# Performance work log

Hardware: AMD Instinct MI355X
Metric: run time of the kernel (lower is better)

The kernel has to match this reference:

```python
import jax, jax.numpy as jnp
import numpy as np
from jax import lax

B, S, D, N, K = 4, 8192, 128, 2, 3
G = N + 1  # n_order + 1 projection groups
EPS_L1 = 1e-8


def _theta(d):
    # RoPE inverse frequencies: 10000^{-2i/d}
    return 1.0 / (10000.0 ** (jnp.arange(d // 2, dtype=jnp.float32) * 2.0 / d))


def _rope(x, pos, theta):
    # x: (B,S,D), pos: (B,S) int -> dimension-wise 2x2 rotations
    ang = pos[..., None].astype(jnp.float32) * theta  # (B,S,D/2)
    c, s = jnp.cos(ang), jnp.sin(ang)
    xe, xo = x[..., 0::2], x[..., 1::2]
    return jnp.stack([xe * c - xo * s, xe * s + xo * c], axis=-1).reshape(x.shape)


def _layernorm(x, g, b, eps=1e-5):
    mu = jnp.mean(x, axis=-1, keepdims=True)
    var = jnp.var(x, axis=-1, keepdims=True)
    return (x - mu) / jnp.sqrt(var + eps) * g + b


def _fft_long_conv(v, h):
    # torch norm='forward': rfft divides by n, irfft does not -> circular conv / (2L)
    L = v.shape[-1]
    n = 2 * L
    V = jnp.fft.rfft(v, n=n, norm='forward')
    H = jnp.fft.rfft(h, n=n, norm='forward')
    return jnp.fft.irfft(V * H, n=n, norm='forward')[..., :L]


def setup_inputs() -> dict:
    key = jax.random.key(0)
    ks = jax.random.split(key, 8)
    sc = lambda fan_in: (2.0 / fan_in) ** 0.5
    return {
        'embeddings': jax.random.normal(ks[0], (B, S, D), dtype=jnp.float32),
        'W_proj': jax.random.normal(ks[1], (D, G * D), dtype=jnp.float32) * sc(D),
        'conv_w': jax.random.normal(ks[2], (G * D, 1, K), dtype=jnp.float32) * sc(K),
        'conv_b': jnp.zeros((G * D,), dtype=jnp.float32),
        'W1': jax.random.normal(ks[3], (D, D), dtype=jnp.float32) * sc(D),
        'b1': jnp.zeros((D,), dtype=jnp.float32),
        'ln_g': jnp.ones((D,), dtype=jnp.float32),
        'ln_b': jnp.zeros((D,), dtype=jnp.float32),
        'W2': jax.random.normal(ks[4], (D, N * D), dtype=jnp.float32) * sc(D),
        'b2': jnp.zeros((N * D,), dtype=jnp.float32),
        'ff_scale': jnp.ones((1, 1, N * D), dtype=jnp.float32),
        'out_proj': jax.random.normal(ks[5], (D, D), dtype=jnp.float32) * sc(D),
        'B_param': jax.random.normal(ks[6], (N, 1, D, 1), dtype=jnp.float32) * sc(D),
        'positions': (jnp.arange(B * S, dtype=jnp.int32).reshape(B, S) % S),
    }


def reference(embeddings, W_proj, conv_w, conv_b, W1, b1, ln_g, ln_b, W2, b2,
              ff_scale, out_proj, B_param, positions):
    theta = _theta(D)
    # --- HyenaProjection: dense proj + fully-depthwise short conv ---
    x = embeddings @ W_proj                      # (B,S,G*D)
    xc = jnp.transpose(x, (0, 2, 1))             # (B,G*D,S)
    z = lax.conv_general_dilated(
        xc, conv_w, (1,), [(K // 2, K // 2)],
        dimension_numbers=('NCH', 'OIH', 'NCH'),
        feature_group_count=G * D) + conv_b[None, :, None]
    # faithful to torch: (B,S,G*D) row-major reshape into (B,D,G,S)
    z = jnp.transpose(z, (0, 2, 1)).reshape(B, D, G, S)
    z_list = [z[:, :, i, :] for i in range(G)]   # each (B,D,S)
    # --- HyenaFilter: RoPE + FFN + L1 normalization over emb dim ---
    t = _rope(embeddings, positions, theta)
    hmid = jax.nn.gelu(_layernorm(t @ W1 + b1, ln_g, ln_b), approximate=False)
    h_hat = (hmid @ W2 + b2) * ff_scale          # (B,S,N*D)
    h_hat = jnp.transpose(h_hat.reshape(B, S, N, D), (0, 2, 3, 1))  # (B,N,D,S)
    h_hat = h_hat / (jnp.sum(jnp.abs(h_hat), axis=-2, keepdims=True) + EPS_L1)
    # --- Hyena recurrence with FFT long conv ---
    v = z_list[-1]
    for i in range(N):
        v = z_list[i] * (_fft_long_conv(v, h_hat[:, i]) + B_param[i] * v)
    out = jnp.transpose(v, (0, 2, 1)) @ out_proj  # (B,S,D)
    return out
```

## Files before the change

### kernel.cpp

```cpp
#include <hip/hip_runtime.h>
#include <hip/hip_bf16.h>
#include <cstdint>

#define BB 4
#define SS 8192
#define DD 128

#define N_EMB  4194304
#define N_WP   49152
#define N_CW   1152
#define N_CB   384
#define N_W1   16384
#define N_B1   128
#define N_LNG  128
#define N_LNB  128
#define N_W2   32768
#define N_B2   256
#define N_FFS  256
#define N_WO   16384
#define N_BP   256
#define N_FINP 4311680

typedef short bf16x8 __attribute__((ext_vector_type(8)));
typedef float f32x4  __attribute__((ext_vector_type(4)));

__device__ __forceinline__ void bfsplit(float v, unsigned short& h, unsigned short& l)
{
    __hip_bfloat16 hb = __float2bfloat16(v);
    float hf = __bfloat162float(hb);
    __hip_bfloat16 lb = __float2bfloat16(v - hf);
    h = *(unsigned short*)&hb;
    l = *(unsigned short*)&lb;
}

__device__ __forceinline__ void packAB(const float* __restrict__ src, bf16x8& H, bf16x8& L)
{
    float4 x0 = *(const float4*)(src);
    float4 x1 = *(const float4*)(src + 4);
    float xv[8] = {x0.x, x0.y, x0.z, x0.w, x1.x, x1.y, x1.z, x1.w};
    unsigned short h[8], l[8];
    #pragma unroll
    for (int j = 0; j < 8; ++j) bfsplit(xv[j], h[j], l[j]);
    #pragma unroll
    for (int j = 0; j < 8; ++j) { H[j] = (short)h[j]; L[j] = (short)l[j]; }
}

struct SrcPtrs { const void* p[13]; };

__device__ __forceinline__ float readf(const void* p, int idx, bool isbf)
{
    if (isbf) return __uint_as_float(((unsigned)((const unsigned short*)p)[idx]) << 16);
    return ((const float*)p)[idx];
}

__global__ __launch_bounds__(256) void k_convert(
    SrcPtrs sp, float* __restrict__ dst,
    unsigned short* __restrict__ embh, unsigned short* __restrict__ embl,
    unsigned short* __restrict__ wpth, unsigned short* __restrict__ wptl,
    unsigned short* __restrict__ w1th, unsigned short* __restrict__ w1tl,
    unsigned short* __restrict__ w2th, unsigned short* __restrict__ w2tl,
    unsigned short* __restrict__ woth, unsigned short* __restrict__ wotl)
{
    static const int sizes[13] = {N_EMB, N_WP, N_CW, N_CB, N_W1, N_B1, N_LNG,
                                  N_LNB, N_W2, N_B2, N_FFS, N_WO, N_BP};
    const unsigned probe = *(const unsigned*)sp.p[6];
    const bool isbf = (probe != 0x3F800000u);
    const int gid = blockIdx.x * 256 + threadIdx.x;
    const int stride = gridDim.x * 256;
    int off = 0;
    for (int seg = 0; seg < 13; ++seg) {
        const int n = sizes[seg];
        float* d = dst + off;
        for (int i = gid; i < n; i += stride) {
            float v = readf(sp.p[seg], i, isbf);
            d[i] = v;
            if (seg == 0) { unsigned short h, l; bfsplit(v, h, l); embh[i] = h; embl[i] = l; }
        }
        off += n;
    }
    for (int i = gid; i < N_WP; i += stride) {
        int n = i >> 7, k = i & 127;
        unsigned short h, l; bfsplit(readf(sp.p[1], k * 384 + n, isbf), h, l);
        wpth[i] = h; wptl[i] = l;
    }
    for (int i = gid; i < N_W1; i += stride) {
        int n = i >> 7, k = i & 127;
        unsigned short h, l; bfsplit(readf(sp.p[4], k * 128 + n, isbf), h, l);
        w1th[i] = h; w1tl[i] = l;
    }
    for (int i = gid; i < N_W2; i += stride) {
        int n = i >> 7, k = i & 127;
        unsigned short h, l; bfsplit(readf(sp.p[8], k * 256 + n, isbf), h, l);
        w2th[i] = h; w2tl[i] = l;
    }
    for (int i = gid; i < N_WO; i += stride) {
        int n = i >> 7, k = i & 127;
        unsigned short h, l; bfsplit(readf(sp.p[11], k * 128 + n, isbf), h, l);
        woth[i] = h; wotl[i] = l;
    }
}

#define PCROWS 112

__global__ __launch_bounds__(512) void k_projconv(
    const unsigned short* __restrict__ embh,
    const unsigned short* __restrict__ embl,
    const unsigned short* __restrict__ wpth,
    const unsigned short* __restrict__ wptl,
    const float* __restrict__ cw,
    const float* __restrict__ cb,
    float* __restrict__ zbuf)
{
    __shared__ float xs[128][68];

    const int b    = blockIdx.y;
    const int s0   = blockIdx.x * PCROWS;
    const int t    = threadIdx.x;
    const int wv   = t >> 6;
    const int lane = t & 63;
    const int m    = lane & 15;
    const int q    = lane >> 4;

    bf16x8 Ah[4], Al[4];
    {
        int sx  = s0 - 8 + 16 * wv + m;
        int sxc = min(max(sx, 0), SS - 1);
        const size_t rowoff = ((size_t)b * SS + sxc) * DD;
        #pragma unroll
        for (int kt = 0; kt < 4; ++kt) {
            int k0 = kt * 32 + q * 8;
            Ah[kt] = *(const bf16x8*)(embh + rowoff + k0);
            Al[kt] = *(const bf16x8*)(embl + rowoff + k0);
        }
    }

    for (int nc = 0; nc < 6; ++nc) {
        #pragma unroll
        for (int nt = 0; nt < 4; ++nt) {
            int n = nc * 64 + nt * 16 + m;
            const size_t noff = (size_t)n * DD;
            f32x4 acc = {0.f, 0.f, 0.f, 0.f};
            #pragma unroll
            for (int kt = 0; kt < 4; ++kt) {
                int k0 = kt * 32 + q * 8;
                bf16x8 Bh = *(const bf16x8*)(wpth + noff + k0);
                bf16x8 Bl = *(const bf16x8*)(wptl + noff + k0);
                acc = __builtin_amdgcn_mfma_f32_16x16x32_bf16(Ah[kt], Bh, acc, 0, 0, 0);
                acc = __builtin_amdgcn_mfma_f32_16x16x32_bf16(Ah[kt], Bl, acc, 0, 0, 0);
                acc = __builtin_amdgcn_mfma_f32_16x16x32_bf16(Al[kt], Bh, acc, 0, 0, 0);
            }
            #pragma unroll
            for (int rg = 0; rg < 4; ++rg)
                xs[16 * wv + 4 * q + rg][nt * 16 + m] = acc[rg];
        }
        __syncthreads();
        {
            int c = t & 63, rg = t >> 6;
            int ch = nc * 64 + c;
            float w0 = cw[ch * 3 + 0], w1 = cw[ch * 3 + 1], w2 = cw[ch * 3 + 2];
            float bias = cb[ch];
            #pragma unroll
            for (int i = 0; i < 14; ++i) {
                int r = rg + 8 * i;
                int s = s0 + r;
                if (s < SS) {
                    float x0 = (s > 0)      ? xs[r + 7][c] : 0.f;
                    float x1 = xs[r + 8][c];
                    float x2 = (s < SS - 1) ? xs[r + 9][c] : 0.f;
                    zbuf[((size_t)b * SS + s) * 384 + ch] = x0 * w0 + x1 * w1 + x2 * w2 + bias;
                }
            }
        }
        __syncthreads();
    }
}

__global__ __launch_bounds__(256) void k_mlp(
    const float* __restrict__ emb,
    const int* __restrict__ positions,
    const unsigned short* __restrict__ w1th,
    const unsigned short* __restrict__ w1tl,
    const float* __restrict__ b1,
    const float* __restrict__ ln_g,
    const float* __restrict__ ln_b,
    const unsigned short* __restrict__ w2th,
    const unsigned short* __restrict__ w2tl,
    const float* __restrict__ b2,
    const float* __restrict__ ffs,
    float* __restrict__ hhat)
{
    const int b  = blockIdx.y;
    const int s0 = blockIdx.x * 16;
    const int t  = threadIdx.x;
    __shared__ float tls[16][132];
    __shared__ float hls[16][132];
    __shared__ float hh[16][257];
    __shared__ float rstat[16][2];

    for (int idx = t; idx < 16 * 64; idx += 256) {
        int r = idx >> 6, i = idx & 63;
        int s = s0 + r;
        const float2 p = ((const float2*)(emb + ((size_t)b * SS + s) * DD))[i];
        float xe = p.x, xo = p.y;
        float pos = (float)positions[(size_t)b * SS + s];
        float th = exp2f((float)i * (-13.287712379549449f / 64.0f));
        float ang = pos * th;
        float sn, cs;
        sincosf(ang, &sn, &cs);
        tls[r][2 * i]     = xe * cs - xo * sn;
        tls[r][2 * i + 1] = xe * sn + xo * cs;
    }
    __syncthreads();

    const int wv = t >> 6, lane = t & 63, m = lane & 15, q = lane >> 4;

    {
        bf16x8 Ah[4], Al[4];
        #pragma unroll
        for (int kt = 0; kt < 4; ++kt)
            packAB(&tls[m][kt * 32 + q * 8], Ah[kt], Al[kt]);
        #pragma unroll
        for (int ntl = 0; ntl < 2; ++ntl) {
            int nt = 2 * wv + ntl;
            int col = nt * 16 + m;
            const size_t noff = (size_t)col * 128;
            f32x4 acc = {0.f, 0.f, 0.f, 0.f};
            #pragma unroll
            for (int kt = 0; kt < 4; ++kt) {
                int k0 = kt * 32 + q * 8;
                bf16x8 Bh = *(const bf16x8*)(w1th + noff + k0);
                bf16x8 Bl = *(const bf16x8*)(w1tl + noff + k0);
                acc = __builtin_amdgcn_mfma_f32_16x16x32_bf16(Ah[kt], Bh, acc, 0, 0, 0);
                acc = __builtin_amdgcn_mfma_f32_16x16x32_bf16(Ah[kt], Bl, acc, 0, 0, 0);
                acc = __builtin_amdgcn_mfma_f32_16x16x32_bf16(Al[kt], Bh, acc, 0, 0, 0);
            }
            float bias = b1[col];
            #pragma unroll
            for (int rg = 0; rg < 4; ++rg)
                hls[4 * q + rg][col] = acc[rg] + bias;
        }
    }
    __syncthreads();

    {
        for (int r = wv; r < 16; r += 4) {
            float x0 = hls[r][lane], x1 = hls[r][lane + 64];
            float sum = x0 + x1, ssq = x0 * x0 + x1 * x1;
            #pragma unroll
            for (int off = 32; off > 0; off >>= 1) {
                sum += __shfl_xor(sum, off);
                ssq += __shfl_xor(ssq, off);
            }
            float mu  = sum * (1.0f / 128.0f);
            float var = ssq * (1.0f / 128.0f) - mu * mu;
            float inv = rsqrtf(var + 1e-5f);
            float y0 = (x0 - mu) * inv * ln_g[lane]      + ln_b[lane];
            float y1 = (x1 - mu) * inv * ln_g[lane + 64] + ln_b[lane + 64];
            hls[r][lane]      = y0 * 0.5f * (1.0f + erff(y0 * 0.70710678118654752f));
            hls[r][lane + 64] = y1 * 0.5f * (1.0f + erff(y1 * 0.70710678118654752f));
        }
    }
    __syncthreads();

    {
        bf16x8 Ah[4], Al[4];
        #pragma unroll
        for (int kt = 0; kt < 4; ++kt)
            packAB(&hls[m][kt * 32 + q * 8], Ah[kt], Al[kt]);
        #pragma unroll
        for (int ntl = 0; ntl < 4; ++ntl) {
            int nt = 4 * wv + ntl;
            int col = nt * 16 + m;
            const size_t noff = (size_t)col * 128;
            f32x4 acc = {0.f, 0.f, 0.f, 0.f};
            #pragma unroll
            for (int kt = 0; kt < 4; ++kt) {
                int k0 = kt * 32 + q * 8;
                bf16x8 Bh = *(const bf16x8*)(w2th + noff + k0);
                bf16x8 Bl = *(const bf16x8*)(w2tl + noff + k0);
                acc = __builtin_amdgcn_mfma_f32_16x16x32_bf16(Ah[kt], Bh, acc, 0, 0, 0);
                acc = __builtin_amdgcn_mfma_f32_16x16x32_bf16(Ah[kt], Bl, acc, 0, 0, 0);
                acc = __builtin_amdgcn_mfma_f32_16x16x32_bf16(Al[kt], Bh, acc, 0, 0, 0);
            }
            float bias = b2[col];
            float fsc  = ffs[col];
            #pragma unroll
            for (int rg = 0; rg < 4; ++rg)
                hh[4 * q + rg][col] = (acc[rg] + bias) * fsc;
        }
    }
    __syncthreads();

    {
        for (int g = wv; g < 32; g += 4) {
            int r = g >> 1, n = g & 1;
            float a = fabsf(hh[r][n * 128 + lane]) + fabsf(hh[r][n * 128 + lane + 64]);
            #pragma unroll
            for (int off = 32; off > 0; off >>= 1) a += __shfl_xor(a, off);
            if (lane == 0) rstat[r][n] = 1.0f / (a + 1e-8f);
        }
    }
    __syncthreads();

    for (int idx = t; idx < 16 * 256; idx += 256) {
        int nd = idx >> 4, rr = idx & 15;
        int n = nd >> 7;
        float val = hh[rr][nd] * rstat[rr][n];
        hhat[((size_t)(b * 2 + n) * 128 + (nd & 127)) * SS + (s0 + rr)] = val;
    }
}

__device__ __forceinline__ int SK(int x) { return x + (x >> 5); }

__global__ __launch_bounds__(1024) void k_fftconv(
    const float* __restrict__ zbuf,
    const float* __restrict__ hhat,
    const float* __restrict__ Bp,
    float* __restrict__ vout)
{
    const int d = blockIdx.x;
    const int b = blockIdx.y;
    const int t = threadIdx.x;
    __shared__ float lre[4224];
    __shared__ float lim[4224];
    __shared__ float2 twF[1280];

    const float c8 = 0.923879532511287f, s8 = 0.382683432365090f, c4 = 0.707106781186548f;

    {
        const int lhs_c[5] = {9, 7, 5, 3, 1};
        for (int idx = t; idx < 1280; idx += 1024) {
            int si = idx >> 8, jj = idx & 255;
            float sn, cs;
            sincospif((float)jj * (-1.0f / (float)(1 << lhs_c[si])), &sn, &cs);
            twF[idx] = make_float2(cs, sn);
        }
    }

    const float* zb = zbuf + (size_t)b * (SS * 384);
    const float* v0 = zb + ((size_t)d * 3 + 2) * SS;
    float vr[8];
    #pragma unroll
    for (int j = 0; j < 8; ++j) vr[j] = v0[t + j * 1024];

    float cre[16], cim[16];
    const float sc = 1.0f / 536870912.0f;
    const int blk = t >> 8, w = t & 255;
    __syncthreads();

    for (int it = 0; it < 2; ++it) {
        const float* hp = hhat + (((size_t)b * 2 + it) * 128 + d) * SS;
        #pragma unroll
        for (int j = 0; j < 8; ++j) { cre[j] = vr[j]; cim[j] = hp[t + j * 1024]; }

        {
            float W0i, W0r; sincospif((float)t * (-1.0f / 8192.0f), &W0i, &W0r);
            const float wjr[4] = {1.f, c8, c4, s8};
            const float wji[4] = {0.f, -s8, -c4, -c8};
            #pragma unroll
            for (int j = 0; j < 4; ++j) {
                float Wr = W0r * wjr[j] - W0i * wji[j];
                float Wi = W0r * wji[j] + W0i * wjr[j];
                float W2r = Wr * Wr - Wi * Wi, W2i = 2.f * Wr * Wi;
                float W3r = W2r * Wr - W2i * Wi, W3i = W2r * Wi + W2i * Wr;
                float a0r = cre[j], a0i = cim[j], a1r = cre[j + 4], a1i = cim[j + 4];
                cre[j] = a0r + a1r; cim[j] = a0i + a1i;
                float dr = a0r - a1r, di = a0i - a1i;
                cre[j + 4] = W2r * dr - W2i * di; cim[j + 4] = W2r * di + W2i * dr;
                float e2r = a0r + a1i, e2i = a0i - a1r;
                cre[j + 8] = Wr * e2r - Wi * e2i; cim[j + 8] = Wr * e2i + Wi * e2r;
                float e3r = a0r - a1i, e3i = a0i + a1r;
                cre[j + 12] = W3r * e3r - W3i * e3i; cim[j + 12] = W3r * e3i + W3i * e3r;
            }
        }
        {
            float Wi, Wr; sincospif((float)t * (-1.0f / 2048.0f), &Wi, &Wr);
            float W2r = Wr * Wr - Wi * Wi, W2i = 2.f * Wr * Wi;
            float W3r = W2r * Wr - W2i * Wi, W3i = W2r * Wi + W2i * Wr;
            #pragma unroll
            for (int g = 0; g < 16; g += 4) {
                float a0r = cre[g], a0i = cim[g], a1r = cre[g + 1], a1i = cim[g + 1];
                float a2r = cre[g + 2], a2i = cim[g + 2], a3r = cre[g + 3], a3i = cim[g + 3];
                float s02r = a0r + a2r, s02i = a0i + a2i, d02r = a0r - a2r, d02i = a0i - a2i;
                float s13r = a1r + a3r, s13i = a1i + a3i, d13r = a1r - a3r, d13i = a1i - a3i;
                cre[g] = s02r + s13r; cim[g] = s02i + s13i;
                float u1r = s02r - s13r, u1i = s02i - s13i;
                cre[g + 1] = W2r * u1r - W2i * u1i; cim[g + 1] = W2r * u1i + W2i * u1r;
                float e2r = d02r + d13i, e2i = d02i - d13r;
                cre[g + 2] = Wr * e2r - Wi * e2i; cim[g + 2] = Wr * e2i + Wi * e2r;
                float e3r = d02r - d13i, e3i = d02i + d13r;
                cre[g + 3] = W3r * e3r - W3i * e3i; cim[g + 3] = W3r * e3i + W3i * e3r;
            }
        }
        #pragma unroll
        for (int p = 0; p < 4; ++p) {
            #pragma unroll
            for (int q = 0; q < 4; ++q) {
                int a = SK(q * 1024 + t);
                lre[a] = cre[4 * p + q]; lim[a] = cim[4 * p + q];
            }
            __syncthreads();
            const int lhs_c[5] = {9, 7, 5, 3, 1};
            #pragma unroll
            for (int si = 0; si < 5; ++si) {
                const int lh = lhs_c[si];
                const int hh = 1 << lh, h2 = hh >> 1;
                const int jj = w & (h2 - 1);
                const int i0 = blk * 1024 + ((w >> (lh - 1)) << (lh + 1)) + jj;
                const float2 wv = twF[si * 256 + jj];
                const float Wr = wv.x, Wi = wv.y;
                const int p0 = SK(i0), p1 = SK(i0 + h2), p2 = SK(i0 + hh), p3 = SK(i0 + hh + h2);
                float a0r = lre[p0], a0i = lim[p0];
                float a1r = lre[p1], a1i = lim[p1];
                float a2r = lre[p2], a2i = lim[p2];
                float a3r = lre[p3], a3i = lim[p3];
                float W2r = Wr * Wr - Wi * Wi, W2i = 2.f * Wr * Wi;
                float W3r = W2r * Wr - W2i * Wi, W3i = W2r * Wi + W2i * Wr;
                float s02r = a0r + a2r, s02i = a0i + a2i, d02r = a0r - a2r, d02i = a0i - a2i;
                float s13r = a1r + a3r, s13i = a1i + a3i, d13r = a1r - a3r, d13i = a1i - a3i;
                lre[p0] = s02r + s13r; lim[p0] = s02i + s13i;
                float u1r = s02r - s13r, u1i = s02i - s13i;
                lre[p1] = W2r * u1r - W2i * u1i; lim[p1] = W2r * u1i + W2i * u1r;
                float e2r = d02r + d13i, e2i = d02i - d13r;
                lre[p2] = Wr * e2r - Wi * e2i; lim[p2] = Wr * e2i + Wi * e2r;
                float e3r = d02r - d13i, e3i = d02i + d13r;
                lre[p3] = W3r * e3r - W3i * e3i; lim[p3] = W3r * e3i + W3i * e3r;
                __syncthreads();
            }
            #pragma unroll
            for (int q = 0; q < 4; ++q) {
                int a = SK(q * 1024 + t);
                cre[4 * p + q] = lre[a]; cim[4 * p + q] = lim[a];
            }
            __syncthreads();
        }

        #pragma unroll
        for (int j = 0; j < 16; ++j) {
            float Cr = cre[j], Ci = cim[j];
            cre[j] = (Cr * Cr - Ci * Ci) * sc;
            cim[j] = 2.0f * Cr * Ci * sc;
        }

        #pragma unroll
        for (int p = 0; p < 4; ++p) {
            #pragma unroll
            for (int q = 0; q < 4; ++q) {
                int a = SK(q * 1024 + t);
                lre[a] = cre[4 * p + q]; lim[a] = cim[4 * p + q];
            }
            __syncthreads();
            const int lqs_c[5] = {0, 2, 4, 6, 8};
            #pragma unroll
            for (int si = 0; si < 5; ++si) {
                const int lq = lqs_c[si];
                const int qv = 1 << lq;
                const int jj = w & (qv - 1);
                const int i0 = blk * 1024 + ((w >> lq) << (lq + 2)) + jj;
                const float2 wv = twF[(4 - si) * 256 + jj];
                const float Wbr = wv.x, Wbi = -wv.y;
                const int p0 = SK(i0), p1 = SK(i0 + qv), p2 = SK(i0 + 2 * qv), p3 = SK(i0 + 3 * qv);
                float a0r = lre[p0], a0i = lim[p0];
                float a1r = lre[p1], a1i = lim[p1];
                float a2r = lre[p2], a2i = lim[p2];
                float a3r = lre[p3], a3i = lim[p3];
                float War = Wbr * Wbr - Wbi * Wbi, Wai = 2.f * Wbr * Wbi;
                float t1r = War * a1r - Wai * a1i, t1i = War * a1i + Wai * a1r;
                float b0r = a0r + t1r, b0i = a0i + t1i, b1r = a0r - t1r, b1i = a0i - t1i;
                float t3r = War * a3r - Wai * a3i, t3i = War * a3i + Wai * a3r;
                float b2r = a2r + t3r, b2i = a2i + t3i, b3r = a2r - t3r, b3i = a2i - t3i;
                float u2r = Wbr * b2r - Wbi * b2i, u2i = Wbr * b2i + Wbi * b2r;
                lre[p0] = b0r + u2r; lim[p0] = b0i + u2i;
                lre[p2] = b0r - u2r; lim[p2] = b0i - u2i;
                float u3r = -Wbi * b3r - Wbr * b3i, u3i = Wbr * b3r - Wbi * b3i;
                lre[p1] = b1r + u3r; lim[p1] = b1i + u3i;
                lre[p3] = b1r - u3r; lim[p3] = b1i - u3i;
                __syncthreads();
            }
            #pragma unroll
            for (int q = 0; q < 4; ++q) {
                int a = SK(q * 1024 + t);
                cre[4 * p + q] = lre[a]; cim[4 * p + q] = lim[a];
            }
            __syncthreads();
        }
        {
            float Wbi, Wbr; sincospif((float)t * (1.0f / 2048.0f), &Wbi, &Wbr);
            float War = Wbr * Wbr - Wbi * Wbi, Wai = 2.f * Wbr * Wbi;
            #pragma unroll
            for (int g = 0; g < 16; g += 4) {
                float a0r = cre[g], a0i = cim[g], a1r = cre[g + 1], a1i = cim[g + 1];
                float a2r = cre[g + 2], a2i = cim[g + 2], a3r = cre[g + 3], a3i = cim[g + 3];
                float t1r = War * a1r - Wai * a1i, t1i = War * a1i + Wai * a1r;
                float b0r = a0r + t1r, b0i = a0i + t1i, b1r = a0r - t1r, b1i = a0i - t1i;
                float t3r = War * a3r - Wai * a3i, t3i = War * a3i + Wai * a3r;
                float b2r = a2r + t3r, b2i = a2i + t3i, b3r = a2r - t3r, b3i = a2i - t3i;
                float u2r = Wbr * b2r - Wbi * b2i, u2i = Wbr * b2i + Wbi * b2r;
                cre[g] = b0r + u2r; cim[g] = b0i + u2i;
                cre[g + 2] = b0r - u2r; cim[g + 2] = b0i - u2i;
                float u3r = -Wbi * b3r - Wbr * b3i, u3i = Wbr * b3r - Wbi * b3i;
                cre[g + 1] = b1r + u3r; cim[g + 1] = b1i + u3i;
                cre[g + 3] = b1r - u3r; cim[g + 3] = b1i - u3i;
            }
        }
        {
            float Bi, Br; sincospif((float)t * (1.0f / 8192.0f), &Bi, &Br);
            const float bjr[4] = {1.f, c8, c4, s8};
            const float bji[4] = {0.f, s8, c4, c8};
            #pragma unroll
            for (int j = 0; j < 4; ++j) {
                float Wbr = Br * bjr[j] - Bi * bji[j];
                float Wbi = Br * bji[j] + Bi * bjr[j];
                float War = Wbr * Wbr - Wbi * Wbi, Wai = 2.f * Wbr * Wbi;
                float a0r = cre[j], a0i = cim[j], a1r = cre[j + 4], a1i = cim[j + 4];
                float a2r = cre[j + 8], a2i = cim[j + 8], a3r = cre[j + 12], a3i = cim[j + 12];
                float t1r = War * a1r - Wai * a1i, t1i = War * a1i + Wai * a1r;
                float b0r = a0r + t1r, b0i = a0i + t1i, b1r = a0r - t1r, b1i = a0i - t1i;
                float t3r = War * a3r - Wai * a3i, t3i = War * a3i + Wai * a3r;
                float b2r = a2r + t3r, b2i = a2i + t3i, b3r = a2r - t3r, b3i = a2i - t3i;
                float u2r = Wbr * b2r - Wbi * b2i, u2i = Wbr * b2i + Wbi * b2r;
                cre[j] = b0r + u2r; cim[j] = b0i + u2i;
                cre[j + 8] = b0r - u2r; cim[j + 8] = b0i - u2i;
                float u3r = -Wbi * b3r - Wbr * b3i, u3i = Wbr * b3r - Wbi * b3i;
                cre[j + 4] = b1r + u3r; cim[j + 4] = b1i + u3i;
                cre[j + 12] = b1r - u3r; cim[j + 12] = b1i - u3i;
            }
        }

        const float* zi = zb + ((size_t)d * 3 + it) * SS;
        const float bpv = Bp[it * 128 + d];
        #pragma unroll
        for (int j = 0; j < 8; ++j) {
            float zz = zi[t + j * 1024];
            vr[j] = zz * (cim[j] + bpv * vr[j]);
        }
        __syncthreads();
    }

    float* vo = vout + ((size_t)b * 128 + d) * SS;
    #pragma unroll
    for (int j = 0; j < 8; ++j) vo[t + j * 1024] = vr[j];
}

__global__ __launch_bounds__(256) void k_outproj(
    const float* __restrict__ vbuf,
    const unsigned short* __restrict__ woth,
    const unsigned short* __restrict__ wotl,
    const unsigned* __restrict__ probe,
    void* __restrict__ outv)
{
    __shared__ float vt[128 * 65];
    const int b  = blockIdx.y;
    const int s0 = blockIdx.x * 64;
    const int t  = threadIdx.x;
    for (int idx = t; idx < 8192; idx += 256) {
        int dd = idx >> 6, sl = idx & 63;
        vt[dd * 65 + sl] = vbuf[((size_t)b * 128 + dd) * SS + s0 + sl];
    }
    const bool isbf = (*probe != 0x3F800000u);
    __syncthreads();

    const int wv = t >> 6, lane = t & 63, m = lane & 15, q = lane >> 4;

    bf16x8 Ah[4], Al[4];
    #pragma unroll
    for (int kt = 0; kt < 4; ++kt) {
        float xv[8];
        unsigned short h[8], l[8];
        #pragma unroll
        for (int j = 0; j < 8; ++j) {
            int dd = kt * 32 + q * 8 + j;
            xv[j] = vt[dd * 65 + 16 * wv + m];
        }
        #pragma unroll
        for (int j = 0; j < 8; ++j) bfsplit(xv[j], h[j], l[j]);
        #pragma unroll
        for (int j = 0; j < 8; ++j) { Ah[kt][j] = (short)h[j]; Al[kt][j] = (short)l[j]; }
    }

    f32x4 acc[8];
    #pragma unroll
    for (int nt = 0; nt < 8; ++nt) {
        acc[nt] = (f32x4){0.f, 0.f, 0.f, 0.f};
        const size_t noff = (size_t)(nt * 16 + m) * 128;
        #pragma unroll
        for (int kt = 0; kt < 4; ++kt) {
            int k0 = kt * 32 + q * 8;
            bf16x8 Bh = *(const bf16x8*)(woth + noff + k0);
            bf16x8 Bl = *(const bf16x8*)(wotl + noff + k0);
            acc[nt] = __builtin_amdgcn_mfma_f32_16x16x32_bf16(Ah[kt], Bh, acc[nt], 0, 0, 0);
            acc[nt] = __builtin_amdgcn_mfma_f32_16x16x32_bf16(Ah[kt], Bl, acc[nt], 0, 0, 0);
            acc[nt] = __builtin_amdgcn_mfma_f32_16x16x32_bf16(Al[kt], Bh, acc[nt], 0, 0, 0);
        }
    }

    if (isbf) {
        __hip_bfloat16* out = (__hip_bfloat16*)outv;
        #pragma unroll
        for (int nt = 0; nt < 8; ++nt)
            #pragma unroll
            for (int rg = 0; rg < 4; ++rg) {
                int s = s0 + 16 * wv + 4 * q + rg;
                out[((size_t)b * SS + s) * DD + nt * 16 + m] = __float2bfloat16(acc[nt][rg]);
            }
    } else {
        float* out = (float*)outv;
        #pragma unroll
        for (int nt = 0; nt < 8; ++nt)
            #pragma unroll
            for (int rg = 0; rg < 4; ++rg) {
                int s = s0 + 16 * wv + 4 * q + rg;
                out[((size_t)b * SS + s) * DD + nt * 16 + m] = acc[nt][rg];
            }
    }
}

extern "C" void kernel_launch(void* const* d_in, const int* in_sizes, int n_in,
                              void* d_out, int out_size, void* d_ws, size_t ws_size,
                              hipStream_t stream)
{
    (void)in_sizes; (void)n_in; (void)out_size; (void)ws_size;
    const int* positions = (const int*)d_in[13];

    float* finp = (float*)d_ws;
    float* zbuf = finp + N_FINP;
    float* hhat = zbuf + (size_t)BB * SS * 384;
    float* vbuf = hhat + (size_t)BB * 2 * 128 * SS;
    unsigned short* embh = (unsigned short*)(vbuf + (size_t)BB * 128 * SS);
    unsigned short* embl = embh + N_EMB;
    unsigned short* wpth = embl + N_EMB;
    unsigned short* wptl = wpth + N_WP;
    unsigned short* w1th = wptl + N_WP;
    unsigned short* w1tl = w1th + N_W1;
    unsigned short* w2th = w1tl + N_W1;
    unsigned short* w2tl = w2th + N_W2;
    unsigned short* woth = w2tl + N_W2;
    unsigned short* wotl = woth + N_WO;

    const float* emb = finp;
    const float* cw  = finp + N_EMB + N_WP;
    const float* cb  = cw  + N_CW;
    const float* b1  = cb  + N_CB + N_W1;
    const float* lng = b1  + N_B1;
    const float* lnb = lng + N_LNG;
    const float* b2  = lnb + N_LNB + N_W2;
    const float* ffs = b2  + N_B2;
    const float* Bp  = ffs + N_FFS + N_WO;

    SrcPtrs sp;
    for (int i = 0; i < 13; ++i) sp.p[i] = d_in[i];

    k_convert<<<dim3(2048), 256, 0, stream>>>(sp, finp, embh, embl, wpth, wptl,
                                              w1th, w1tl, w2th, w2tl, woth, wotl);
    k_projconv<<<dim3((SS + PCROWS - 1) / PCROWS, BB), 512, 0, stream>>>(
        embh, embl, wpth, wptl, cw, cb, zbuf);
    k_mlp<<<dim3(SS / 16, BB), 256, 0, stream>>>(emb, positions, w1th, w1tl, b1,
                                                 lng, lnb, w2th, w2tl, b2, ffs, hhat);
    k_fftconv<<<dim3(DD, BB), 1024, 0, stream>>>(zbuf, hhat, Bp, vbuf);
    k_outproj<<<dim3(SS / 64, BB), 256, 0, stream>>>(vbuf, woth, wotl,
                                                     (const unsigned*)d_in[6], d_out);
}
```

Baseline: 412.1 us.

## Restructure in-block FFT stages as register radix-4 plus wavefront shuffles

Changes the middle FFT stages of the long-convolution kernel. Instead of five LDS radix-4 passes, each with its own barrier, repeated over four chunks, the data is transposed through shared memory once per direction. The remaining stages then run as in-register radix-4 butterflies plus six cross-lane shuffle stages, with twiddles computed per lane by repeated squaring. This removes most LDS traffic, the shared twiddle table and many __syncthreads. In exchange it adds shuffle instructions, divergent branches within each wavefront and more register pressure at 1024 threads per block.

Result: slower. 728.6 us (+76.8%).

```diff
diff --git a/kernel.cpp b/kernel.cpp
--- a/kernel.cpp
+++ b/kernel.cpp
@@ -310,7 +310,8 @@
     }
 }
 
-__device__ __forceinline__ int SK(int x) { return x + (x >> 5); }
+#define SQFLIP(rr_, ii_, flip_) { float _r = rr_*rr_ - ii_*ii_, _i = 2.f*rr_*ii_; \
+    if (flip_) { _r = -_r; _i = -_i; } rr_ = _r; ii_ = _i; }
 
 __global__ __launch_bounds__(1024) void k_fftconv(
     const float* __restrict__ zbuf,
@@ -321,21 +322,11 @@
     const int d = blockIdx.x;
     const int b = blockIdx.y;
     const int t = threadIdx.x;
-    __shared__ float lre[4224];
-    __shared__ float lim[4224];
-    __shared__ float2 twF[1280];
+    const int wv = t >> 6, l = t & 63;
+    __shared__ float tre[4096];
+    __shared__ float tim[4096];
 
     const float c8 = 0.923879532511287f, s8 = 0.382683432365090f, c4 = 0.707106781186548f;
-
-    {
-        const int lhs_c[5] = {9, 7, 5, 3, 1};
-        for (int idx = t; idx < 1280; idx += 1024) {
-            int si = idx >> 8, jj = idx & 255;
-            float sn, cs;
-            sincospif((float)jj * (-1.0f / (float)(1 << lhs_c[si])), &sn, &cs);
-            twF[idx] = make_float2(cs, sn);
-        }
-    }
 
     const float* zb = zbuf + (size_t)b * (SS * 384);
     const float* v0 = zb + ((size_t)d * 3 + 2) * SS;
@@ -343,10 +334,93 @@
     #pragma unroll
     for (int j = 0; j < 8; ++j) vr[j] = v0[t + j * 1024];
 
+    float t32r, t32i; sincospif((float)(l & 31) * (-1.0f / 32.0f), &t32i, &t32r);
+    float t16r = t32r, t16i = t32i; SQFLIP(t16r, t16i, (l & 16));
+    float t8r  = t16r, t8i  = t16i; SQFLIP(t8r,  t8i,  (l & 8));
+    float t4r  = t8r,  t4i  = t8i;  SQFLIP(t4r,  t4i,  (l & 4));
+    float t2r  = t4r,  t2i  = t4i;  SQFLIP(t2r,  t2i,  (l & 2));
+
     float cre[16], cim[16];
     const float sc = 1.0f / 536870912.0f;
-    const int blk = t >> 8, w = t & 255;
-    __syncthreads();
+
+    auto F4F = [&](int i0a, int i1a, int i2a, int i3a, float Wr_, float Wi_) {
+        float W2r = Wr_ * Wr_ - Wi_ * Wi_, W2i = 2.f * Wr_ * Wi_;
+        float W3r = W2r * Wr_ - W2i * Wi_, W3i = W2r * Wi_ + W2i * Wr_;
+        float a0r = cre[i0a], a0i = cim[i0a], a1r = cre[i1a], a1i = cim[i1a];
+        float a2r = cre[i2a], a2i = cim[i2a], a3r = cre[i3a], a3i = cim[i3a];
+        float s02r = a0r + a2r, s02i = a0i + a2i, d02r = a0r - a2r, d02i = a0i - a2i;
+        float s13r = a1r + a3r, s13i = a1i + a3i, d13r = a1r - a3r, d13i = a1i - a3i;
+        cre[i0a] = s02r + s13r; cim[i0a] = s02i + s13i;
+        float u1r = s02r - s13r, u1i = s02i - s13i;
+        cre[i1a] = W2r * u1r - W2i * u1i; cim[i1a] = W2r * u1i + W2i * u1r;
+        float e2r = d02r + d13i, e2i = d02i - d13r;
+        cre[i2a] = Wr_ * e2r - Wi_ * e2i; cim[i2a] = Wr_ * e2i + Wi_ * e2r;
+        float e3r = d02r - d13i, e3i = d02i + d13r;
+        cre[i3a] = W3r * e3r - W3i * e3i; cim[i3a] = W3r * e3i + W3i * e3r;
+    };
+    auto F4I = [&](int i0a, int i1a, int i2a, int i3a, float Wbr, float Wbi) {
+        float War = Wbr * Wbr - Wbi * Wbi, Wai = 2.f * Wbr * Wbi;
+        float a0r = cre[i0a], a0i = cim[i0a], a1r = cre[i1a], a1i = cim[i1a];
+        float a2r = cre[i2a], a2i = cim[i2a], a3r = cre[i3a], a3i = cim[i3a];
+        float t1r = War * a1r - Wai * a1i, t1i = War * a1i + Wai * a1r;
+        float b0r = a0r + t1r, b0i = a0i + t1i, b1r = a0r - t1r, b1i = a0i - t1i;
+        float t3r = War * a3r - Wai * a3i, t3i = War * a3i + Wai * a3r;
+        float b2r = a2r + t3r, b2i = a2i + t3i, b3r = a2r - t3r, b3i = a2i - t3i;
+        float u2r = Wbr * b2r - Wbi * b2i, u2i = Wbr * b2i + Wbi * b2r;
+        cre[i0a] = b0r + u2r; cim[i0a] = b0i + u2i;
+        cre[i2a] = b0r - u2r; cim[i2a] = b0i - u2i;
+        float u3r = -Wbi * b3r - Wbr * b3i, u3i = Wbr * b3r - Wbi * b3i;
+        cre[i1a] = b1r + u3r; cim[i1a] = b1i + u3i;
+        cre[i3a] = b1r - u3r; cim[i3a] = b1i - u3i;
+    };
+    auto FSH = [&](int h, float Wr_, float Wi_) {
+        #pragma unroll
+        for (int rr = 0; rr < 16; ++rr) {
+            float pr = __shfl_xor(cre[rr], h);
+            float pi = __shfl_xor(cim[rr], h);
+            if (l & h) {
+                float dr = pr - cre[rr], di = pi - cim[rr];
+                cre[rr] = dr * Wr_ - di * Wi_;
+                cim[rr] = dr * Wi_ + di * Wr_;
+            } else {
+                cre[rr] += pr; cim[rr] += pi;
+            }
+        }
+    };
+    auto ISH = [&](int h, float Wr_, float Wi_) {
+        #pragma unroll
+        for (int rr = 0; rr < 16; ++rr) {
+            float tr, ti;
+            if (l & h) { tr = cre[rr] * Wr_ - cim[rr] * Wi_; ti = cre[rr] * Wi_ + cim[rr] * Wr_; }
+            else       { tr = cre[rr]; ti = cim[rr]; }
+            float pr = __shfl_xor(tr, h);
+            float pi = __shfl_xor(ti, h);
+            cre[rr] = (l & h) ? (pr - tr) : (tr + pr);
+            cim[rr] = (l & h) ? (pi - ti) : (ti + pi);
+        }
+    };
+    auto TRANS = [&]() {
+        #pragma unroll
+        for (int p = 0; p < 4; ++p) {
+            const int lp = l & 15;
+            if ((l >> 4) == p) {
+                #pragma unroll
+                for (int j = 0; j < 16; ++j) {
+                    int a = j * 256 + wv * 16 + lp;
+                    tre[a] = cre[j]; tim[a] = cim[j];
+                }
+            }
+            __syncthreads();
+            if ((l >> 4) == p) {
+                #pragma unroll
+                for (int r = 0; r < 16; ++r) {
+                    int a = wv * 256 + r * 16 + lp;
+                    cre[r] = tre[a]; cim[r] = tim[a];
+                }
+            }
+            __syncthreads();
+        }
+    };
 
     for (int it = 0; it < 2; ++it) {
         const float* hp = hhat + (((size_t)b * 2 + it) * 128 + d) * SS;
@@ -375,65 +449,27 @@
         }
         {
             float Wi, Wr; sincospif((float)t * (-1.0f / 2048.0f), &Wi, &Wr);
-            float W2r = Wr * Wr - Wi * Wi, W2i = 2.f * Wr * Wi;
-            float W3r = W2r * Wr - W2i * Wi, W3i = W2r * Wi + W2i * Wr;
-            #pragma unroll
-            for (int g = 0; g < 16; g += 4) {
-                float a0r = cre[g], a0i = cim[g], a1r = cre[g + 1], a1i = cim[g + 1];
-                float a2r = cre[g + 2], a2i = cim[g + 2], a3r = cre[g + 3], a3i = cim[g + 3];
-                float s02r = a0r + a2r, s02i = a0i + a2i, d02r = a0r - a2r, d02i = a0i - a2i;
-                float s13r = a1r + a3r, s13i = a1i + a3i, d13r = a1r - a3r, d13i = a1i - a3i;
-                cre[g] = s02r + s13r; cim[g] = s02i + s13i;
-                float u1r = s02r - s13r, u1i = s02i - s13i;
-                cre[g + 1] = W2r * u1r - W2i * u1i; cim[g + 1] = W2r * u1i + W2i * u1r;
-                float e2r = d02r + d13i, e2i = d02i - d13r;
-                cre[g + 2] = Wr * e2r - Wi * e2i; cim[g + 2] = Wr * e2i + Wi * e2r;
-                float e3r = d02r - d13i, e3i = d02i + d13r;
-                cre[g + 3] = W3r * e3r - W3i * e3i; cim[g + 3] = W3r * e3i + W3i * e3r;
-            }
-        }
-        #pragma unroll
-        for (int p = 0; p < 4; ++p) {
-            #pragma unroll
-            for (int q = 0; q < 4; ++q) {
-                int a = SK(q * 1024 + t);
-                lre[a] = cre[4 * p + q]; lim[a] = cim[4 * p + q];
-            }
-            __syncthreads();
-            const int lhs_c[5] = {9, 7, 5, 3, 1};
-            #pragma unroll
-            for (int si = 0; si < 5; ++si) {
-                const int lh = lhs_c[si];
-                const int hh = 1 << lh, h2 = hh >> 1;
-                const int jj = w & (h2 - 1);
-                const int i0 = blk * 1024 + ((w >> (lh - 1)) << (lh + 1)) + jj;
-                const float2 wv = twF[si * 256 + jj];
-                const float Wr = wv.x, Wi = wv.y;
-                const int p0 = SK(i0), p1 = SK(i0 + h2), p2 = SK(i0 + hh), p3 = SK(i0 + hh + h2);
-                float a0r = lre[p0], a0i = lim[p0];
-                float a1r = lre[p1], a1i = lim[p1];
-                float a2r = lre[p2], a2i = lim[p2];
-                float a3r = lre[p3], a3i = lim[p3];
-                float W2r = Wr * Wr - Wi * Wi, W2i = 2.f * Wr * Wi;
-                float W3r = W2r * Wr - W2i * Wi, W3i = W2r * Wi + W2i * Wr;
-                float s02r = a0r + a2r, s02i = a0i + a2i, d02r = a0r - a2r, d02i = a0i - a2i;
-                float s13r = a1r + a3r, s13i = a1i + a3i, d13r = a1r - a3r, d13i = a1i - a3i;
-                lre[p0] = s02r + s13r; lim[p0] = s02i + s13i;
-                float u1r = s02r - s13r, u1i = s02i - s13i;
-                lre[p1] = W2r * u1r - W2i * u1i; lim[p1] = W2r * u1i + W2i * u1r;
-                float e2r = d02r + d13i, e2i = d02i - d13r;
-                lre[p2] = Wr * e2r - Wi * e2i; lim[p2] = Wr * e2i + Wi * e2r;
-                float e3r = d02r - d13i, e3i = d02i + d13r;
-                lre[p3] = W3r * e3r - W3i * e3i; lim[p3] = W3r * e3i + W3i * e3r;
-                __syncthreads();
-            }
-            #pragma unroll
-            for (int q = 0; q < 4; ++q) {
-                int a = SK(q * 1024 + t);
-                cre[4 * p + q] = lre[a]; cim[4 * p + q] = lim[a];
-            }
-            __syncthreads();
-        }
+            #pragma unroll
+            for (int g = 0; g < 16; g += 4)
+                F4F(g, g + 1, g + 2, g + 3, Wr, Wi);
+        }
+        TRANS();
+        {
+            float wr, wi; sincospif((float)l * (-1.0f / 512.0f), &wi, &wr);
+            #pragma unroll
+            for (int r = 0; r < 4; ++r) {
+                F4F(r, r + 4, r + 8, r + 12, wr, wi);
+                float nr = wr * c8 - wi * (-s8), ni = wr * (-s8) + wi * c8;
+                wr = nr; wi = ni;
+            }
+        }
+        {
+            float wr, wi; sincospif((float)l * (-1.0f / 128.0f), &wi, &wr);
+            F4F(0, 1, 2, 3, wr, wi);  F4F(4, 5, 6, 7, wr, wi);
+            F4F(8, 9, 10, 11, wr, wi); F4F(12, 13, 14, 15, wr, wi);
+        }
+        FSH(32, t32r, t32i); FSH(16, t16r, t16i); FSH(8, t8r, t8i);
+        FSH(4, t4r, t4i);    FSH(2, t2r, t2i);    FSH(1, 1.f, 0.f);
 
         #pragma unroll
         for (int j = 0; j < 16; ++j) {
@@ -442,66 +478,28 @@
             cim[j] = 2.0f * Cr * Ci * sc;
         }
 
-        #pragma unroll
-        for (int p = 0; p < 4; ++p) {
-            #pragma unroll
-            for (int q = 0; q < 4; ++q) {
-                int a = SK(q * 1024 + t);
-                lre[a] = cre[4 * p + q]; lim[a] = cim[4 * p + q];
-            }
-            __syncthreads();
-            const int lqs_c[5] = {0, 2, 4, 6, 8};
-            #pragma unroll
-            for (int si = 0; si < 5; ++si) {
-                const int lq = lqs_c[si];
-                const int qv = 1 << lq;
-                const int jj = w & (qv - 1);
-                const int i0 = blk * 1024 + ((w >> lq) << (lq + 2)) + jj;
-                const float2 wv = twF[(4 - si) * 256 + jj];
-                const float Wbr = wv.x, Wbi = -wv.y;
-                const int p0 = SK(i0), p1 = SK(i0 + qv), p2 = SK(i0 + 2 * qv), p3 = SK(i0 + 3 * qv);
-                float a0r = lre[p0], a0i = lim[p0];
-                float a1r = lre[p1], a1i = lim[p1];
-                float a2r = lre[p2], a2i = lim[p2];
-                float a3r = lre[p3], a3i = lim[p3];
-                float War = Wbr * Wbr - Wbi * Wbi, Wai = 2.f * Wbr * Wbi;
-                float t1r = War * a1r - Wai * a1i, t1i = War * a1i + Wai * a1r;
-                float b0r = a0r + t1r, b0i = a0i + t1i, b1r = a0r - t1r, b1i = a0i - t1i;
-                float t3r = War * a3r - Wai * a3i, t3i = War * a3i + Wai * a3r;
-                float b2r = a2r + t3r, b2i = a2i + t3i, b3r = a2r - t3r, b3i = a2i - t3i;
-                float u2r = Wbr * b2r - Wbi * b2i, u2i = Wbr * b2i + Wbi * b2r;
-                lre[p0] = b0r + u2r; lim[p0] = b0i + u2i;
-                lre[p2] = b0r - u2r; lim[p2] = b0i - u2i;
-                float u3r = -Wbi * b3r - Wbr * b3i, u3i = Wbr * b3r - Wbi * b3i;
-                lre[p1] = b1r + u3r; lim[p1] = b1i + u3i;
-                lre[p3] = b1r - u3r; lim[p3] = b1i - u3i;
-                __syncthreads();
-            }
-            #pragma unroll
-            for (int q = 0; q < 4; ++q) {
-                int a = SK(q * 1024 + t);
-                cre[4 * p + q] = lre[a]; cim[4 * p + q] = lim[a];
-            }
-            __syncthreads();
-        }
+        ISH(1, 1.f, 0.f);    ISH(2, t2r, -t2i);   ISH(4, t4r, -t4i);
+        ISH(8, t8r, -t8i);   ISH(16, t16r, -t16i); ISH(32, t32r, -t32i);
+        {
+            float wr, wi; sincospif((float)l * (1.0f / 128.0f), &wi, &wr);
+            F4I(0, 1, 2, 3, wr, wi);  F4I(4, 5, 6, 7, wr, wi);
+            F4I(8, 9, 10, 11, wr, wi); F4I(12, 13, 14, 15, wr, wi);
+        }
+        {
+            float wr, wi; sincospif((float)l * (1.0f / 512.0f), &wi, &wr);
+            #pragma unroll
+            for (int r = 0; r < 4; ++r) {
+                F4I(r, r + 4, r + 8, r + 12, wr, wi);
+                float nr = wr * c8 - wi * s8, ni = wr * s8 + wi * c8;
+                wr = nr; wi = ni;
+            }
+        }
+        TRANS();
         {
             float Wbi, Wbr; sincospif((float)t * (1.0f / 2048.0f), &Wbi, &Wbr);
-            float War = Wbr * Wbr - Wbi * Wbi, Wai = 2.f * Wbr * Wbi;
-            #pragma unroll
-            for (int g = 0; g < 16; g += 4) {
-                float a0r = cre[g], a0i = cim[g], a1r = cre[g + 1], a1i = cim[g + 1];
-                float a2r = cre[g + 2], a2i = cim[g + 2], a3r = cre[g + 3], a3i = cim[g + 3];
-                float t1r = War * a1r - Wai * a1i, t1i = War * a1i + Wai * a1r;
-                float b0r = a0r + t1r, b0i = a0i + t1i, b1r = a0r - t1r, b1i = a0i - t1i;
-                float t3r = War * a3r - Wai * a3i, t3i = War * a3i + Wai * a3r;
-                float b2r = a2r + t3r, b2i = a2i + t3i, b3r = a2r - t3r, b3i = a2i - t3i;
-                float u2r = Wbr * b2r - Wbi * b2i, u2i = Wbr * b2i + Wbi * b2r;
-                cre[g] = b0r + u2r; cim[g] = b0i + u2i;
-                cre[g + 2] = b0r - u2r; cim[g + 2] = b0i - u2i;
-                float u3r = -Wbi * b3r - Wbr * b3i, u3i = Wbr * b3r - Wbi * b3i;
-                cre[g + 1] = b1r + u3r; cim[g + 1] = b1i + u3i;
-                cre[g + 3] = b1r - u3r; cim[g + 3] = b1i - u3i;
-            }
+            #pragma unroll
+            for (int g = 0; g < 16; g += 4)
+                F4I(g, g + 1, g + 2, g + 3, Wbr, Wbi);
         }
         {
             float Bi, Br; sincospif((float)t * (1.0f / 8192.0f), &Bi, &Br);
@@ -511,19 +509,7 @@
             for (int j = 0; j < 4; ++j) {
                 float Wbr = Br * bjr[j] - Bi * bji[j];
                 float Wbi = Br * bji[j] + Bi * bjr[j];
-                float War = Wbr * Wbr - Wbi * Wbi, Wai = 2.f * Wbr * Wbi;
-                float a0r = cre[j], a0i = cim[j], a1r = cre[j + 4], a1i = cim[j + 4];
-                float a2r = cre[j + 8], a2i = cim[j + 8], a3r = cre[j + 12], a3i = cim[j + 12];
-                float t1r = War * a1r - Wai * a1i, t1i = War * a1i + Wai * a1r;
-                float b0r = a0r + t1r, b0i = a0i + t1i, b1r = a0r - t1r, b1i = a0i - t1i;
-                float t3r = War * a3r - Wai * a3i, t3i = War * a3i + Wai * a3r;
-                float b2r = a2r + t3r, b2i = a2i + t3i, b3r = a2r - t3r, b3i = a2i - t3i;
-                float u2r = Wbr * b2r - Wbi * b2i, u2i = Wbr * b2i + Wbi * b2r;
-                cre[j] = b0r + u2r; cim[j] = b0i + u2i;
-                cre[j + 8] = b0r - u2r; cim[j + 8] = b0i - u2i;
-                float u3r = -Wbi * b3r - Wbr * b3i, u3i = Wbr * b3r - Wbi * b3i;
-                cre[j + 4] = b1r + u3r; cim[j + 4] = b1i + u3i;
-                cre[j + 12] = b1r - u3r; cim[j + 12] = b1i - u3i;
+                F4I(j, j + 4, j + 8, j + 12, Wbr, Wbi);
             }
         }
 
@@ -534,7 +520,6 @@
             float zz = zi[t + j * 1024];
             vr[j] = zz * (cim[j] + bpv * vr[j]);
         }
-        __syncthreads();
     }
 
     float* vo = vout + ((size_t)b * 128 + d) * SS;
```
